# Kernel optimization log

Hardware: AMD Instinct MI355X
Metric: run time of the kernel (lower is better)

The kernel has to match this reference:

```python
import jax, jax.numpy as jnp
import numpy as np
from jax import lax

INPUT_DIM = 1
HIDDEN_DIM = 256
MAX_SEQ_LEN = 512
BATCH = 8192


def setup_inputs() -> dict:
    key = jax.random.key(0)
    ks = jax.random.split(key, 8)
    s = 1.0 / np.sqrt(HIDDEN_DIM)
    x = jax.random.normal(ks[0], (BATCH, 1, INPUT_DIM), dtype=jnp.float32)
    # torch nn.LSTM params, gate order (i, f, g, o)
    W_ih = jax.random.uniform(ks[1], (4 * HIDDEN_DIM, INPUT_DIM), minval=-s, maxval=s, dtype=jnp.float32)
    W_hh = jax.random.uniform(ks[2], (4 * HIDDEN_DIM, HIDDEN_DIM), minval=-s, maxval=s, dtype=jnp.float32)
    b_ih = jax.random.uniform(ks[3], (4 * HIDDEN_DIM,), minval=-s, maxval=s, dtype=jnp.float32)
    b_hh = jax.random.uniform(ks[4], (4 * HIDDEN_DIM,), minval=-s, maxval=s, dtype=jnp.float32)
    W_fc = jax.random.uniform(ks[5], (1, HIDDEN_DIM), minval=-s, maxval=s, dtype=jnp.float32)
    b_fc = jax.random.uniform(ks[6], (1,), minval=-s, maxval=s, dtype=jnp.float32)
    return {"x": x, "W_ih": W_ih, "W_hh": W_hh, "b_ih": b_ih, "b_hh": b_hh,
            "W_fc": W_fc, "b_fc": b_fc, "max_seq_len": MAX_SEQ_LEN}


def reference(x, W_ih, W_hh, b_ih, b_hh, W_fc, b_fc, max_seq_len):
    B = x.shape[0]
    H = W_hh.shape[1]
    b = b_ih + b_hh  # fold biases once

    def step(carry, _):
        h, c, inp = carry                      # h,c: [B,H]; inp: [B,1]
        gates = inp @ W_ih.T + h @ W_hh.T + b  # [B,4H]
        i, f, g, o = jnp.split(gates, 4, axis=-1)
        c = jax.nn.sigmoid(f) * c + jax.nn.sigmoid(i) * jnp.tanh(g)
        h = jax.nn.sigmoid(o) * jnp.tanh(c)
        d = h @ W_fc.T + b_fc                  # [B,1] depth marker (fc + squeeze of seq dim)
        # torch: outputs[-1].detach() is fed back as next input
        return (h, c, lax.stop_gradient(d)), d

    h0 = jnp.zeros((B, H), dtype=x.dtype)
    c0 = jnp.zeros((B, H), dtype=x.dtype)
    inp0 = x[:, 0, :]                          # [B, input_dim=1]
    _, ds = lax.scan(step, (h0, c0, inp0), None, length=max_seq_len)  # [T,B,1]
    return jnp.moveaxis(ds, 0, 1)              # [B,T,1] == torch.stack(outputs, dim=1)
```

## Files before the change

### kernel.cpp

```cpp
#include <hip/hip_runtime.h>
#include <math.h>

#define HID   256
#define TLEN  512
#define NTHR  1024
#define GSIZE 8
#define NGRP  32
#define BBG   256

#define PLANE_U16 (16 * 8 * 512)
#define HEX_U16   ((size_t)NGRP * 2 * 2 * PLANE_U16)
#define FLAGS_OFF (HEX_U16 * 2)
#define NFLAGS    (NGRP * GSIZE)
#define WS_NEEDED (FLAGS_OFF + (size_t)NFLAGS * 4)

typedef __attribute__((ext_vector_type(8))) short short8;
typedef __attribute__((ext_vector_type(4))) float f32x4;

typedef union {
    float4 f;
    uint4  u;
    short8 s;
} v16u;

static __device__ __forceinline__ unsigned short f2bf_rne(float x) {
    unsigned int u = __float_as_uint(x);
    unsigned int r = (u + 0x7FFFu + ((u >> 16) & 1u)) >> 16;
    return (unsigned short)r;
}
static __device__ __forceinline__ float sigf(float x) {
    return 1.0f / (1.0f + __expf(-x));
}
static __device__ __forceinline__ float tanhf_fast(float x) {
    return 1.0f - 2.0f / (1.0f + __expf(2.0f * x));
}

static __device__ __forceinline__ void issue_dev(const void* p, float4& a) {
    asm volatile("global_load_dwordx4 %0, %1, off sc0 sc1"
                 : "=&v"(a) : "v"(p) : "memory");
}
static __device__ __forceinline__ void store_short_dev(void* p, unsigned int v) {
    asm volatile("global_store_short %0, %1, off sc0 sc1"
                 :: "v"(p), "v"(v) : "memory");
}
static __device__ __forceinline__ unsigned int load_flag_dev(const unsigned int* p) {
    unsigned int v;
    asm volatile("global_load_dword %0, %1, off sc0 sc1\n\t"
                 "s_waitcnt vmcnt(0)"
                 : "=v"(v) : "v"(p) : "memory");
    return v;
}
static __device__ __forceinline__ void store_flag_dev(unsigned int* p, unsigned int v) {
    asm volatile("global_store_dword %0, %1, off sc0 sc1"
                 :: "v"(p), "v"(v) : "memory");
}

__global__ void init_flags(unsigned int* flags) {
    int i = blockIdx.x * 256 + threadIdx.x;
    if (i < NFLAGS) store_flag_dev(flags + i, 0u);
}

__global__ __launch_bounds__(NTHR, 4) void lstm_coop8(
    const float* __restrict__ x,
    const float* __restrict__ W_ih,
    const float* __restrict__ W_hh,
    const float* __restrict__ b_ih,
    const float* __restrict__ b_hh,
    const float* __restrict__ W_fc,
    const float* __restrict__ b_fc,
    unsigned short* __restrict__ hexw,
    unsigned int* __restrict__ flags,
    float* __restrict__ out)
{
    const int tid  = threadIdx.x;
    const int bid  = blockIdx.x;
    const int xcd  = bid & 7;
    const int p    = (bid >> 3) & 7;
    const int gsub = bid >> 6;
    const int g    = xcd * 4 + gsub;
    const int bbase = g * BBG;
    const int mt   = tid >> 6;
    const int lane = tid & 63;
    const int l15  = lane & 15;
    const int l4   = lane >> 4;

    __shared__ unsigned short whi_s[64 * 512];
    __shared__ unsigned short wlo_s[64 * 512];
    __shared__ unsigned short fhi_s[8 * 512];
    __shared__ unsigned short flo_s[8 * 512];
    __shared__ float wfc_s[HID];

    #pragma unroll
    for (int i = 0; i < 4; ++i) {
        int tile = mt * 4 + i;
        int nt = tile >> 3, kc = tile & 7;
        int q = nt >> 1, half = nt & 1;
        int grow = q * 256 + p * 32 + half * 16 + l15;
        int k0 = kc * 32 + l4 * 8;
        const float* src = W_hh + (size_t)grow * HID + k0;
        float4 wa = *(const float4*)src;
        float4 wb = *(const float4*)(src + 4);
        float ff[8] = {wa.x, wa.y, wa.z, wa.w, wb.x, wb.y, wb.z, wb.w};
        short8 hi8, lo8;
        #pragma unroll
        for (int e = 0; e < 8; ++e) {
            unsigned int u = __float_as_uint(ff[e]);
            hi8[e] = (short)(u >> 16);
            float res = ff[e] - __uint_as_float(u & 0xffff0000u);
            lo8[e] = (short)f2bf_rne(res);
        }
        *(short8*)&whi_s[tile * 512 + lane * 8] = hi8;
        *(short8*)&wlo_s[tile * 512 + lane * 8] = lo8;
    }
    if (mt < 8) {
        int kc = mt;
        short8 fh = {0,0,0,0,0,0,0,0};
        short8 fl = {0,0,0,0,0,0,0,0};
        if (l15 == 0) {
            #pragma unroll
            for (int e = 0; e < 8; ++e) {
                float wv = W_fc[kc * 32 + l4 * 8 + e];
                unsigned int u = __float_as_uint(wv);
                fh[e] = (short)(u >> 16);
                float res = wv - __uint_as_float(u & 0xffff0000u);
                fl[e] = (short)f2bf_rne(res);
            }
        }
        *(short8*)&fhi_s[kc * 512 + lane * 8] = fh;
        *(short8*)&flo_s[kc * 512 + lane * 8] = fl;
    }
    if (tid < HID) wfc_s[tid] = W_fc[tid];

    float biasv[8], wihv[8];
    #pragma unroll
    for (int nt = 0; nt < 8; ++nt) {
        int grow = (nt >> 1) * 256 + p * 32 + (nt & 1) * 16 + l15;
        biasv[nt] = b_ih[grow] + b_hh[grow];
        wihv[nt]  = W_ih[grow];
    }
    const float bfc = b_fc[0];

    float c_r[2][4];
    #pragma unroll
    for (int half = 0; half < 2; ++half)
        #pragma unroll
        for (int r = 0; r < 4; ++r) c_r[half][r] = 0.0f;

    unsigned int* flg = flags + g * GSIZE;
    unsigned short* const gbase = hexw + (size_t)g * 4 * PLANE_U16;

    __syncthreads();

    {
        float dreg[4];
        #pragma unroll
        for (int r = 0; r < 4; ++r) dreg[r] = x[bbase + mt * 16 + l4 * 4 + r];

        unsigned short* hiw = gbase + (1 * 2 + 0) * PLANE_U16;
        unsigned short* low = gbase + (1 * 2 + 1) * PLANE_U16;
        #pragma unroll
        for (int half = 0; half < 2; ++half) {
            #pragma unroll
            for (int r = 0; r < 4; ++r) {
                float gi = fmaf(dreg[r], wihv[0 + half], biasv[0 + half]);
                float gf = fmaf(dreg[r], wihv[2 + half], biasv[2 + half]);
                float gg = fmaf(dreg[r], wihv[4 + half], biasv[4 + half]);
                float go = fmaf(dreg[r], wihv[6 + half], biasv[6 + half]);
                float c = fmaf(sigf(gf), c_r[half][r], sigf(gi) * tanhf_fast(gg));
                c_r[half][r] = c;
                float h = sigf(go) * tanhf_fast(c);
                int lane_d = l4 * 4 + r + 16 * (half * 2 + (l15 >> 3));
                int idx = (mt * 8 + p) * 512 + lane_d * 8 + (l15 & 7);
                unsigned int u = __float_as_uint(h);
                store_short_dev(hiw + idx, u >> 16);
                float res = h - __uint_as_float(u & 0xffff0000u);
                store_short_dev(low + idx, (unsigned int)f2bf_rne(res));
            }
        }
        asm volatile("s_waitcnt vmcnt(0)" ::: "memory");
        __syncthreads();
        if (tid == 0) store_flag_dev(&flg[p], 1u);
    }

    #pragma unroll 1
    for (int t = 1; t < TLEN; ++t) {
        if (tid < GSIZE) {
            int guard = 0;
            while (load_flag_dev(&flg[tid]) < (unsigned int)t) {
                if (++guard > (1 << 18)) break;
            }
        }
        __syncthreads();

        const unsigned short* hir = gbase + ((t & 1) * 2 + 0) * PLANE_U16
                                  + (mt * 8) * 512 + lane * 8;
        const unsigned short* lor = gbase + ((t & 1) * 2 + 1) * PLANE_U16
                                  + (mt * 8) * 512 + lane * 8;

        f32x4 acc[8];
        #pragma unroll
        for (int nt = 0; nt < 8; ++nt)
            #pragma unroll
            for (int r = 0; r < 4; ++r) acc[nt][r] = 0.0f;
        f32x4 accd = {0.0f, 0.0f, 0.0f, 0.0f};

        v16u pfh[3], pfl[3];
        issue_dev(hir, pfh[0].f);
        issue_dev(lor, pfl[0].f);
        issue_dev(hir + 512, pfh[1].f);
        issue_dev(lor + 512, pfl[1].f);

        #pragma unroll
        for (int kc = 0; kc < 8; ++kc) {
            if (kc < 6) {
                issue_dev(hir + (kc + 2) * 512, pfh[(kc + 2) % 3].f);
                issue_dev(lor + (kc + 2) * 512, pfl[(kc + 2) % 3].f);
                asm volatile("s_waitcnt vmcnt(4)" ::: "memory");
            } else if (kc == 6) {
                asm volatile("s_waitcnt vmcnt(2)" ::: "memory");
            } else {
                asm volatile("s_waitcnt vmcnt(0)" ::: "memory");
            }
            __builtin_amdgcn_sched_barrier(0);

            const v16u ha = pfh[kc % 3];
            const v16u la = pfl[kc % 3];

            #pragma unroll
            for (int nt = 0; nt < 8; ++nt) {
                short8 bhi = *(const short8*)&whi_s[(nt * 8 + kc) * 512 + lane * 8];
                short8 blo = *(const short8*)&wlo_s[(nt * 8 + kc) * 512 + lane * 8];
                acc[nt] = __builtin_amdgcn_mfma_f32_16x16x32_bf16(ha.s, bhi, acc[nt], 0, 0, 0);
                acc[nt] = __builtin_amdgcn_mfma_f32_16x16x32_bf16(la.s, bhi, acc[nt], 0, 0, 0);
                acc[nt] = __builtin_amdgcn_mfma_f32_16x16x32_bf16(ha.s, blo, acc[nt], 0, 0, 0);
            }
            {
                short8 fh = *(const short8*)&fhi_s[kc * 512 + lane * 8];
                short8 fl = *(const short8*)&flo_s[kc * 512 + lane * 8];
                accd = __builtin_amdgcn_mfma_f32_16x16x32_bf16(ha.s, fh, accd, 0, 0, 0);
                accd = __builtin_amdgcn_mfma_f32_16x16x32_bf16(la.s, fh, accd, 0, 0, 0);
                accd = __builtin_amdgcn_mfma_f32_16x16x32_bf16(ha.s, fl, accd, 0, 0, 0);
            }
        }

        if (p == 0 && l15 == 0) {
            #pragma unroll
            for (int r = 0; r < 4; ++r)
                out[(size_t)(bbase + mt * 16 + l4 * 4 + r) * TLEN + (t - 1)] = accd[r] + bfc;
        }
        float dreg[4];
        #pragma unroll
        for (int r = 0; r < 4; ++r)
            dreg[r] = __shfl(accd[r], lane & 48) + bfc;

        unsigned short* hiw = gbase + ((((t + 1) & 1)) * 2 + 0) * PLANE_U16;
        unsigned short* low = gbase + ((((t + 1) & 1)) * 2 + 1) * PLANE_U16;
        #pragma unroll
        for (int half = 0; half < 2; ++half) {
            #pragma unroll
            for (int r = 0; r < 4; ++r) {
                float gi = acc[0 + half][r] + fmaf(dreg[r], wihv[0 + half], biasv[0 + half]);
                float gf = acc[2 + half][r] + fmaf(dreg[r], wihv[2 + half], biasv[2 + half]);
                float gg = acc[4 + half][r] + fmaf(dreg[r], wihv[4 + half], biasv[4 + half]);
                float go = acc[6 + half][r] + fmaf(dreg[r], wihv[6 + half], biasv[6 + half]);
                float c = fmaf(sigf(gf), c_r[half][r], sigf(gi) * tanhf_fast(gg));
                c_r[half][r] = c;
                float h = sigf(go) * tanhf_fast(c);
                int lane_d = l4 * 4 + r + 16 * (half * 2 + (l15 >> 3));
                int idx = (mt * 8 + p) * 512 + lane_d * 8 + (l15 & 7);
                unsigned int u = __float_as_uint(h);
                store_short_dev(hiw + idx, u >> 16);
                float res = h - __uint_as_float(u & 0xffff0000u);
                store_short_dev(low + idx, (unsigned int)f2bf_rne(res));
            }
        }
        asm volatile("s_waitcnt vmcnt(0)" ::: "memory");
        __syncthreads();
        if (tid == 0) store_flag_dev(&flg[p], (unsigned int)(t + 1));
    }

    {
        if (tid < GSIZE) {
            int guard = 0;
            while (load_flag_dev(&flg[tid]) < (unsigned int)TLEN) {
                if (++guard > (1 << 18)) break;
            }
        }
        __syncthreads();
        if (p == 0) {
            const unsigned short* hir = gbase + (0 * 2 + 0) * PLANE_U16
                                      + (mt * 8) * 512 + lane * 8;
            const unsigned short* lor = gbase + (0 * 2 + 1) * PLANE_U16
                                      + (mt * 8) * 512 + lane * 8;
            float dsum = 0.0f;
            #pragma unroll
            for (int kc = 0; kc < 8; ++kc) {
                v16u va, vb;
                issue_dev(hir + kc * 512, va.f);
                issue_dev(lor + kc * 512, vb.f);
                asm volatile("s_waitcnt vmcnt(0)" ::: "memory");
                __builtin_amdgcn_sched_barrier(0);
                const float* wf = &wfc_s[kc * 32 + l4 * 8];
                unsigned int uu[4] = {va.u.x, va.u.y, va.u.z, va.u.w};
                unsigned int ll[4] = {vb.u.x, vb.u.y, vb.u.z, vb.u.w};
                #pragma unroll
                for (int i = 0; i < 4; ++i) {
                    float h0 = __uint_as_float(uu[i] << 16)
                             + __uint_as_float(ll[i] << 16);
                    float h1 = __uint_as_float(uu[i] & 0xffff0000u)
                             + __uint_as_float(ll[i] & 0xffff0000u);
                    dsum = fmaf(h0, wf[2 * i + 0], dsum);
                    dsum = fmaf(h1, wf[2 * i + 1], dsum);
                }
            }
            dsum += __shfl_xor(dsum, 16);
            dsum += __shfl_xor(dsum, 32);
            if (lane < 16)
                out[(size_t)(bbase + mt * 16 + lane) * TLEN + (TLEN - 1)] = dsum + bfc;
        }
    }
}

#define BB 32
__global__ __launch_bounds__(NTHR, 4) void lstm_mfma7(
    const float* __restrict__ x, const float* __restrict__ W_ih,
    const float* __restrict__ W_hh, const float* __restrict__ b_ih,
    const float* __restrict__ b_hh, const float* __restrict__ W_fc,
    const float* __restrict__ b_fc, float* __restrict__ out)
{
    const int tid = threadIdx.x;
    const int wave = tid >> 6;
    const int lane = tid & 63;
    const int l15 = lane & 15;
    const int l4 = lane >> 4;
    const int bbase = blockIdx.x * BB;

    __shared__ unsigned short hhi[2][16 * 512];
    __shared__ unsigned short hlo[2][16 * 512];
    __shared__ float dpart[16][BB];
    __shared__ float inp_s[BB];

    for (int i = tid; i < 16 * 512; i += NTHR) { hhi[0][i] = 0; hlo[0][i] = 0; }
    if (tid < BB) inp_s[tid] = x[bbase + tid];

    float biasv[4], wihv[4];
    #pragma unroll
    for (int q = 0; q < 4; ++q) {
        int gg = 256 * q + 16 * wave + l15;
        biasv[q] = b_ih[gg] + b_hh[gg];
        wihv[q] = W_ih[gg];
    }
    const float wfc = W_fc[16 * wave + l15];
    const float bfc = b_fc[0];
    const float* __restrict__ wrow = W_hh + (size_t)(16 * wave + l15) * HID + l4 * 8;
    const int kc_w = wave >> 1;
    const int kwhi = (wave & 1) * 2 + (l15 >> 3);
    const int elemw = l15 & 7;

    float c_r[2][4];
    #pragma unroll
    for (int m = 0; m < 2; ++m)
        #pragma unroll
        for (int r = 0; r < 4; ++r) c_r[m][r] = 0.0f;
    __syncthreads();

    #pragma unroll 1
    for (int t = 0; t < TLEN; ++t) {
        const int p = t & 1;
        f32x4 acc[2][4];
        {
            float dv[2][4];
            #pragma unroll
            for (int m = 0; m < 2; ++m)
                #pragma unroll
                for (int r = 0; r < 4; ++r) dv[m][r] = inp_s[16 * m + 4 * l4 + r];
            #pragma unroll
            for (int m = 0; m < 2; ++m)
                #pragma unroll
                for (int q = 0; q < 4; ++q)
                    #pragma unroll
                    for (int r = 0; r < 4; ++r)
                        acc[m][q][r] = fmaf(dv[m][r], wihv[q], biasv[q]);
        }
        #pragma unroll
        for (int kc = 0; kc < 8; ++kc) {
            short8 ahi[2], alo[2];
            #pragma unroll
            for (int m = 0; m < 2; ++m) {
                int aoff = (m * 8 + kc) * 512 + lane * 8;
                ahi[m] = *(const short8*)&hhi[p][aoff];
                alo[m] = *(const short8*)&hlo[p][aoff];
            }
            #pragma unroll
            for (int q = 0; q < 4; ++q) {
                const float* src = wrow + (size_t)q * 256 * HID + kc * 32;
                float4 wa = *(const float4*)src;
                float4 wb = *(const float4*)(src + 4);
                float ff[8] = {wa.x, wa.y, wa.z, wa.w, wb.x, wb.y, wb.z, wb.w};
                short8 bhi, blo;
                #pragma unroll
                for (int e = 0; e < 8; ++e) {
                    unsigned int u = __float_as_uint(ff[e]);
                    bhi[e] = (short)(u >> 16);
                    float res = ff[e] - __uint_as_float(u & 0xffff0000u);
                    blo[e] = (short)(__float_as_uint(res) >> 16);
                }
                #pragma unroll
                for (int m = 0; m < 2; ++m) {
                    acc[m][q] = __builtin_amdgcn_mfma_f32_16x16x32_bf16(ahi[m], bhi, acc[m][q], 0, 0, 0);
                    acc[m][q] = __builtin_amdgcn_mfma_f32_16x16x32_bf16(alo[m], bhi, acc[m][q], 0, 0, 0);
                    acc[m][q] = __builtin_amdgcn_mfma_f32_16x16x32_bf16(ahi[m], blo, acc[m][q], 0, 0, 0);
                }
            }
        }
        #pragma unroll
        for (int m = 0; m < 2; ++m) {
            #pragma unroll
            for (int r = 0; r < 4; ++r) {
                float gi = acc[m][0][r];
                float gf = acc[m][1][r];
                float gg = acc[m][2][r];
                float go = acc[m][3][r];
                float c = fmaf(sigf(gf), c_r[m][r], sigf(gi) * tanhf_fast(gg));
                c_r[m][r] = c;
                float h = sigf(go) * tanhf_fast(c);
                unsigned short hh = f2bf_rne(h);
                float hres = h - __uint_as_float(__float_as_uint(h) & 0xffff0000u);
                int haddr = (m * 8 + kc_w) * 512 + ((4 * l4 + r) + 16 * kwhi) * 8 + elemw;
                hhi[p ^ 1][haddr] = hh;
                hlo[p ^ 1][haddr] = f2bf_rne(hres);
                float s = h * wfc;
                s += __shfl_xor(s, 1);
                s += __shfl_xor(s, 2);
                s += __shfl_xor(s, 4);
                s += __shfl_xor(s, 8);
                if (l15 == 0) dpart[wave][16 * m + 4 * l4 + r] = s;
            }
        }
        __syncthreads();
        if (tid < BB) {
            float s = bfc;
            #pragma unroll
            for (int w = 0; w < 16; ++w) s += dpart[w][tid];
            inp_s[tid] = s;
            out[(size_t)(bbase + tid) * TLEN + t] = s;
        }
        __syncthreads();
    }
}

extern "C" void kernel_launch(void* const* d_in, const int* in_sizes, int n_in,
                              void* d_out, int out_size, void* d_ws, size_t ws_size,
                              hipStream_t stream) {
    const float* x    = (const float*)d_in[0];
    const float* W_ih = (const float*)d_in[1];
    const float* W_hh = (const float*)d_in[2];
    const float* b_ih = (const float*)d_in[3];
    const float* b_hh = (const float*)d_in[4];
    const float* W_fc = (const float*)d_in[5];
    const float* b_fc = (const float*)d_in[6];
    float* out = (float*)d_out;

    const int BATCH = in_sizes[0];

    if (ws_size >= WS_NEEDED) {
        unsigned int* flags = (unsigned int*)((char*)d_ws + FLAGS_OFF);
        init_flags<<<1, 256, 0, stream>>>(flags);
        lstm_coop8<<<BATCH / BBG * GSIZE, NTHR, 0, stream>>>(
            x, W_ih, W_hh, b_ih, b_hh, W_fc, b_fc,
            (unsigned short*)d_ws, flags, out);
    } else {
        lstm_mfma7<<<BATCH / BB, NTHR, 0, stream>>>(
            x, W_ih, W_hh, b_ih, b_hh, W_fc, b_fc, out);
    }
}
```

Before: 7.848 ms.

## Replace block-wide barriers with per-wavefront flag synchronization across cooperating blocks

Each wavefront (indexed by mt) now owns its own set of 8 cross-block flags per group, and publishes and polls them directly. This removes the two __syncthreads per timestep and the single-thread flag store/poll. Wavefronts handling different batch rows can then advance independently instead of waiting for the whole 1024-thread block. The cost is 16x more flags and many more concurrent polling loads on the L2/global path, which could add memory contention.

```diff
diff --git a/kernel.cpp b/kernel.cpp
--- a/kernel.cpp
+++ b/kernel.cpp
@@ -11,7 +11,7 @@
 #define PLANE_U16 (16 * 8 * 512)
 #define HEX_U16   ((size_t)NGRP * 2 * 2 * PLANE_U16)
 #define FLAGS_OFF (HEX_U16 * 2)
-#define NFLAGS    (NGRP * GSIZE)
+#define NFLAGS    (NGRP * 16 * 8)
 #define WS_NEEDED (FLAGS_OFF + (size_t)NFLAGS * 4)
 
 typedef __attribute__((ext_vector_type(8))) short short8;
@@ -60,7 +60,7 @@
     if (i < NFLAGS) store_flag_dev(flags + i, 0u);
 }
 
-__global__ __launch_bounds__(NTHR, 4) void lstm_coop8(
+__global__ __launch_bounds__(NTHR, 4) void lstm_coop9(
     const float* __restrict__ x,
     const float* __restrict__ W_ih,
     const float* __restrict__ W_hh,
@@ -146,7 +146,7 @@
         #pragma unroll
         for (int r = 0; r < 4; ++r) c_r[half][r] = 0.0f;
 
-    unsigned int* flg = flags + g * GSIZE;
+    unsigned int* flg = flags + (g * 16 + mt) * 8;
     unsigned short* const gbase = hexw + (size_t)g * 4 * PLANE_U16;
 
     __syncthreads();
@@ -178,19 +178,20 @@
             }
         }
         asm volatile("s_waitcnt vmcnt(0)" ::: "memory");
-        __syncthreads();
-        if (tid == 0) store_flag_dev(&flg[p], 1u);
+        if (lane == 0) store_flag_dev(&flg[p], 1u);
     }
 
     #pragma unroll 1
     for (int t = 1; t < TLEN; ++t) {
-        if (tid < GSIZE) {
+        {
             int guard = 0;
-            while (load_flag_dev(&flg[tid]) < (unsigned int)t) {
+            for (;;) {
+                unsigned int v = (unsigned int)t;
+                if (lane < 8) v = load_flag_dev(&flg[lane]);
+                if (__all(v >= (unsigned int)t)) break;
                 if (++guard > (1 << 18)) break;
             }
         }
-        __syncthreads();
 
         const unsigned short* hir = gbase + ((t & 1) * 2 + 0) * PLANE_U16
                                   + (mt * 8) * 512 + lane * 8;
@@ -275,18 +276,19 @@
             }
         }
         asm volatile("s_waitcnt vmcnt(0)" ::: "memory");
-        __syncthreads();
-        if (tid == 0) store_flag_dev(&flg[p], (unsigned int)(t + 1));
+        if (lane == 0) store_flag_dev(&flg[p], (unsigned int)(t + 1));
     }
 
     {
-        if (tid < GSIZE) {
+        {
             int guard = 0;
-            while (load_flag_dev(&flg[tid]) < (unsigned int)TLEN) {
+            for (;;) {
+                unsigned int v = (unsigned int)TLEN;
+                if (lane < 8) v = load_flag_dev(&flg[lane]);
+                if (__all(v >= (unsigned int)TLEN)) break;
                 if (++guard > (1 << 18)) break;
             }
         }
-        __syncthreads();
         if (p == 0) {
             const unsigned short* hir = gbase + (0 * 2 + 0) * PLANE_U16
                                       + (mt * 8) * 512 + lane * 8;
@@ -465,8 +467,8 @@
 
     if (ws_size >= WS_NEEDED) {
         unsigned int* flags = (unsigned int*)((char*)d_ws + FLAGS_OFF);
-        init_flags<<<1, 256, 0, stream>>>(flags);
-        lstm_coop8<<<BATCH / BBG * GSIZE, NTHR, 0, stream>>>(
+        init_flags<<<(NFLAGS + 255) / 256, 256, 0, stream>>>(flags);
+        lstm_coop9<<<BATCH / BBG * GSIZE, NTHR, 0, stream>>>(
             x, W_ih, W_hh, b_ih, b_hh, W_fc, b_fc,
             (unsigned short*)d_ws, flags, out);
     } else {
```

Result: slower. 9.251 ms (+17.9%).

## Assign cooperative groups by hardware XCD id and use L2-scope h exchange

Applied to the files above, without the earlier changes.

Each block now reads its XCC_ID register and takes a slot from a per-XCD atomic counter, so the 8 blocks of each cooperative group are guaranteed to run on the same XCD instead of relying on the dispatch order implied by blockIdx. The hidden-state exchange loads and stores then drop the sc1 bit and use L2 (sc0) scope, avoiding system/device-coherent traffic that crosses XCDs. This targets the per-timestep synchronisation latency between the 8 blocks of a group. The risk is a correctness failure if more than 32 blocks land on one XCD or if slot assignment differs from the assumed layout, because the &31 wrap would then cause slot collisions.

```diff
diff --git a/kernel.cpp b/kernel.cpp
--- a/kernel.cpp
+++ b/kernel.cpp
@@ -12,7 +12,8 @@
 #define HEX_U16   ((size_t)NGRP * 2 * 2 * PLANE_U16)
 #define FLAGS_OFF (HEX_U16 * 2)
 #define NFLAGS    (NGRP * GSIZE)
-#define WS_NEEDED (FLAGS_OFF + (size_t)NFLAGS * 4)
+#define CNT_OFF   (FLAGS_OFF + (size_t)NFLAGS * 4)
+#define WS_NEEDED (CNT_OFF + 8 * 4)
 
 typedef __attribute__((ext_vector_type(8))) short short8;
 typedef __attribute__((ext_vector_type(4))) float f32x4;
@@ -35,12 +36,12 @@
     return 1.0f - 2.0f / (1.0f + __expf(2.0f * x));
 }
 
-static __device__ __forceinline__ void issue_dev(const void* p, float4& a) {
-    asm volatile("global_load_dwordx4 %0, %1, off sc0 sc1"
+static __device__ __forceinline__ void issue_l2(const void* p, float4& a) {
+    asm volatile("global_load_dwordx4 %0, %1, off sc0"
                  : "=&v"(a) : "v"(p) : "memory");
 }
-static __device__ __forceinline__ void store_short_dev(void* p, unsigned int v) {
-    asm volatile("global_store_short %0, %1, off sc0 sc1"
+static __device__ __forceinline__ void store_short_l2(void* p, unsigned int v) {
+    asm volatile("global_store_short %0, %1, off sc0"
                  :: "v"(p), "v"(v) : "memory");
 }
 static __device__ __forceinline__ unsigned int load_flag_dev(const unsigned int* p) {
@@ -55,12 +56,13 @@
                  :: "v"(p), "v"(v) : "memory");
 }
 
-__global__ void init_flags(unsigned int* flags) {
+__global__ void init_flags(unsigned int* flags, unsigned int* cnt) {
     int i = blockIdx.x * 256 + threadIdx.x;
     if (i < NFLAGS) store_flag_dev(flags + i, 0u);
-}
-
-__global__ __launch_bounds__(NTHR, 4) void lstm_coop8(
+    if (i < 8) store_flag_dev(cnt + i, 0u);
+}
+
+__global__ __launch_bounds__(NTHR, 4) void lstm_coop11(
     const float* __restrict__ x,
     const float* __restrict__ W_ih,
     const float* __restrict__ W_hh,
@@ -70,15 +72,10 @@
     const float* __restrict__ b_fc,
     unsigned short* __restrict__ hexw,
     unsigned int* __restrict__ flags,
+    unsigned int* __restrict__ xcnt,
     float* __restrict__ out)
 {
     const int tid  = threadIdx.x;
-    const int bid  = blockIdx.x;
-    const int xcd  = bid & 7;
-    const int p    = (bid >> 3) & 7;
-    const int gsub = bid >> 6;
-    const int g    = xcd * 4 + gsub;
-    const int bbase = g * BBG;
     const int mt   = tid >> 6;
     const int lane = tid & 63;
     const int l15  = lane & 15;
@@ -89,6 +86,20 @@
     __shared__ unsigned short fhi_s[8 * 512];
     __shared__ unsigned short flo_s[8 * 512];
     __shared__ float wfc_s[HID];
+    __shared__ int slot_s;
+
+    if (tid == 0) {
+        unsigned int myxcd;
+        asm volatile("s_getreg_b32 %0, hwreg(HW_REG_XCC_ID)" : "=s"(myxcd));
+        myxcd &= 7u;
+        unsigned int s = atomicAdd(&xcnt[myxcd], 1u) & 31u;
+        slot_s = (int)(myxcd * 32u + s);
+    }
+    __syncthreads();
+    const int slot = slot_s;
+    const int g    = slot >> 3;
+    const int p    = slot & 7;
+    const int bbase = g * BBG;
 
     #pragma unroll
     for (int i = 0; i < 4; ++i) {
@@ -172,9 +183,9 @@
                 int lane_d = l4 * 4 + r + 16 * (half * 2 + (l15 >> 3));
                 int idx = (mt * 8 + p) * 512 + lane_d * 8 + (l15 & 7);
                 unsigned int u = __float_as_uint(h);
-                store_short_dev(hiw + idx, u >> 16);
+                store_short_l2(hiw + idx, u >> 16);
                 float res = h - __uint_as_float(u & 0xffff0000u);
-                store_short_dev(low + idx, (unsigned int)f2bf_rne(res));
+                store_short_l2(low + idx, (unsigned int)f2bf_rne(res));
             }
         }
         asm volatile("s_waitcnt vmcnt(0)" ::: "memory");
@@ -205,16 +216,16 @@
         f32x4 accd = {0.0f, 0.0f, 0.0f, 0.0f};
 
         v16u pfh[3], pfl[3];
-        issue_dev(hir, pfh[0].f);
-        issue_dev(lor, pfl[0].f);
-        issue_dev(hir + 512, pfh[1].f);
-        issue_dev(lor + 512, pfl[1].f);
+        issue_l2(hir, pfh[0].f);
+        issue_l2(lor, pfl[0].f);
+        issue_l2(hir + 512, pfh[1].f);
+        issue_l2(lor + 512, pfl[1].f);
 
         #pragma unroll
         for (int kc = 0; kc < 8; ++kc) {
             if (kc < 6) {
-                issue_dev(hir + (kc + 2) * 512, pfh[(kc + 2) % 3].f);
-                issue_dev(lor + (kc + 2) * 512, pfl[(kc + 2) % 3].f);
+                issue_l2(hir + (kc + 2) * 512, pfh[(kc + 2) % 3].f);
+                issue_l2(lor + (kc + 2) * 512, pfl[(kc + 2) % 3].f);
                 asm volatile("s_waitcnt vmcnt(4)" ::: "memory");
             } else if (kc == 6) {
                 asm volatile("s_waitcnt vmcnt(2)" ::: "memory");
@@ -269,9 +280,9 @@
                 int lane_d = l4 * 4 + r + 16 * (half * 2 + (l15 >> 3));
                 int idx = (mt * 8 + p) * 512 + lane_d * 8 + (l15 & 7);
                 unsigned int u = __float_as_uint(h);
-                store_short_dev(hiw + idx, u >> 16);
+                store_short_l2(hiw + idx, u >> 16);
                 float res = h - __uint_as_float(u & 0xffff0000u);
-                store_short_dev(low + idx, (unsigned int)f2bf_rne(res));
+                store_short_l2(low + idx, (unsigned int)f2bf_rne(res));
             }
         }
         asm volatile("s_waitcnt vmcnt(0)" ::: "memory");
@@ -296,8 +307,8 @@
             #pragma unroll
             for (int kc = 0; kc < 8; ++kc) {
                 v16u va, vb;
-                issue_dev(hir + kc * 512, va.f);
-                issue_dev(lor + kc * 512, vb.f);
+                issue_l2(hir + kc * 512, va.f);
+                issue_l2(lor + kc * 512, vb.f);
                 asm volatile("s_waitcnt vmcnt(0)" ::: "memory");
                 __builtin_amdgcn_sched_barrier(0);
                 const float* wf = &wfc_s[kc * 32 + l4 * 8];
@@ -465,10 +476,11 @@
 
     if (ws_size >= WS_NEEDED) {
         unsigned int* flags = (unsigned int*)((char*)d_ws + FLAGS_OFF);
-        init_flags<<<1, 256, 0, stream>>>(flags);
-        lstm_coop8<<<BATCH / BBG * GSIZE, NTHR, 0, stream>>>(
+        unsigned int* xcnt  = (unsigned int*)((char*)d_ws + CNT_OFF);
+        init_flags<<<1, 256, 0, stream>>>(flags, xcnt);
+        lstm_coop11<<<BATCH / BBG * GSIZE, NTHR, 0, stream>>>(
             x, W_ih, W_hh, b_ih, b_hh, W_fc, b_fc,
-            (unsigned short*)d_ws, flags, out);
+            (unsigned short*)d_ws, flags, xcnt, out);
     } else {
         lstm_mfma7<<<BATCH / BB, NTHR, 0, stream>>>(
             x, W_ih, W_hh, b_ih, b_hh, W_fc, b_fc, out);
```

Result: faster. 7.068 ms (median of 2 runs) (-9.9%).
